# Kernel optimization log

Hardware: AMD Instinct MI355X
Metric: run time of the kernel (lower is better)

Reference implementation:

```python
import jax, jax.numpy as jnp
import numpy as np

B, S, D = 8, 2048, 2048          # batch, seq, hidden
E, K, NSTEPS = 16, 2, 4          # routed experts, top_k, routers
NSH = 2                          # shared experts
DR = D // 4                      # routed inner dim (routed_ratio=4)
DS = D // 2                      # shared inner dim (shared_ratio=2)


def setup_inputs() -> dict:
    key = jax.random.key(0)
    ks = jax.random.split(key, 8)
    s = 0.02
    return {
        "x": jax.random.normal(ks[0], (B, S, D), jnp.float32),
        "step_t": 1,
        "router_w": jax.random.normal(ks[1], (NSTEPS, D, E), jnp.float32) * s,
        "re_w1": jax.random.normal(ks[2], (E, D, DR), jnp.float32) * s,
        "re_b1": jnp.zeros((E, DR), jnp.float32),
        "re_w2": jax.random.normal(ks[3], (E, DR, D), jnp.float32) * s,
        "re_b2": jnp.zeros((E, D), jnp.float32),
        "sh_w1": jax.random.normal(ks[4], (NSH, D, DS), jnp.float32) * s,
        "sh_b1": jnp.zeros((NSH, DS), jnp.float32),
        "sh_w2": jax.random.normal(ks[5], (NSH, DS, D), jnp.float32) * s,
        "sh_b2": jnp.zeros((NSH, D), jnp.float32),
    }


def reference(x, step_t, router_w, re_w1, re_b1, re_w2, re_b2, sh_w1, sh_b1, sh_w2, sh_b2):
    orig = x.shape
    flat = x.reshape(-1, orig[-1])                       # [T, D]
    T = flat.shape[0]

    # shared expert group: sum of always-active experts
    h = jax.nn.silu(jnp.einsum('td,sdk->tsk', flat, sh_w1) + sh_b1)   # [T, NSH, DS]
    out = jnp.einsum('tsk,skd->td', h, sh_w2) + sh_b2.sum(0)          # [T, D]

    # top-k router for this step (eval mode: no jitter noise)
    logits = flat @ router_w[step_t]                     # [T, E]
    probs = jax.nn.softmax(logits, axis=-1)
    w, idx = jax.lax.top_k(probs, K)                     # [T, K]

    # combine weights per (token, expert): sum_k w_k * 1[idx_k == e]
    cw = jnp.zeros((T, E), flat.dtype).at[jnp.arange(T)[:, None], idx].add(w)

    # routed experts: masked gather-compute-scatter expressed as
    # weighted accumulation (zero combine-weight == token not routed)
    def body(acc, p):
        w1, b1, w2, b2, cwe = p                          # cwe: [T]
        ye = jax.nn.silu(flat @ w1 + b1) @ w2 + b2       # [T, D]
        return acc + cwe[:, None] * ye, None

    out, _ = jax.lax.scan(body, out, (re_w1, re_b1, re_w2, re_b2, cw.T))
    return out.reshape(orig)
```

## Files before the change

kernel.cpp:

```cpp
#include <hip/hip_runtime.h>
#include <hip/hip_bf16.h>
#include <stdint.h>


#define DEV static __device__ __forceinline__

typedef __attribute__((ext_vector_type(8))) short bf16x8;
typedef __attribute__((ext_vector_type(4))) float f32x4;

constexpr int T_TOK = 16384;
constexpr int DIM   = 2048;
constexpr int NEXP  = 16;
constexpr int DR_K  = 512;
constexpr int DS_K  = 1024;
constexpr int MAXROWS = 34816;
constexpr int MAXTILES = 272;

DEV void gload16(const void* g, void* l) {
  __builtin_amdgcn_global_load_lds(
      (const __attribute__((address_space(1))) unsigned int*)g,
      (__attribute__((address_space(3))) unsigned int*)l, 16, 0, 0);
}

DEV float silu_f(float v) { return v / (1.f + __expf(-v)); }

__global__ __launch_bounds__(256) void cast_router_kernel(
    const float* __restrict__ x, __hip_bfloat16* __restrict__ xb,
    const float* __restrict__ rw_all, const int* __restrict__ step_p,
    int* __restrict__ tk_idx, float* __restrict__ tk_w) {
  int tid = threadIdx.x;
  int t0 = blockIdx.x * 8;
  __shared__ float xs[8][1024];
  __shared__ float red[4][4][8][4];

  float acc[8][4];
#pragma unroll
  for (int tk = 0; tk < 8; ++tk)
#pragma unroll
    for (int j = 0; j < 4; ++j) acc[tk][j] = 0.f;

  const float* rwbase = rw_all + (size_t)step_p[0] * DIM * NEXP;

#pragma unroll
  for (int half = 0; half < 2; ++half) {
#pragma unroll
    for (int tk = 0; tk < 8; ++tk) {
      const float4* xp = (const float4*)(x + (size_t)(t0 + tk) * DIM + half * 1024);
      float4 v = xp[tid];
      *(float4*)&xs[tk][tid * 4] = v;
      union { ushort4 u; __hip_bfloat16 h[4]; } o;
      o.h[0] = __float2bfloat16(v.x); o.h[1] = __float2bfloat16(v.y);
      o.h[2] = __float2bfloat16(v.z); o.h[3] = __float2bfloat16(v.w);
      *(ushort4*)(xb + (size_t)(t0 + tk) * DIM + half * 1024 + tid * 4) = o.u;
    }
    __syncthreads();
    const float4* rw4 = (const float4*)(rwbase + (size_t)half * 1024 * NEXP);
#pragma unroll 4
    for (int i = 0; i < 16; ++i) {
      int c = i * 256 + tid;
      int d = c >> 2;
      float4 wv = rw4[c];
#pragma unroll
      for (int tk = 0; tk < 8; ++tk) {
        float v = xs[tk][d];
        acc[tk][0] += v * wv.x; acc[tk][1] += v * wv.y;
        acc[tk][2] += v * wv.z; acc[tk][3] += v * wv.w;
      }
    }
    __syncthreads();
  }

#pragma unroll
  for (int m = 4; m < 64; m <<= 1) {
#pragma unroll
    for (int tk = 0; tk < 8; ++tk) {
      acc[tk][0] += __shfl_xor(acc[tk][0], m);
      acc[tk][1] += __shfl_xor(acc[tk][1], m);
      acc[tk][2] += __shfl_xor(acc[tk][2], m);
      acc[tk][3] += __shfl_xor(acc[tk][3], m);
    }
  }
  int lane = tid & 63, wvi = tid >> 6;
  if (lane < 4) {
#pragma unroll
    for (int tk = 0; tk < 8; ++tk) {
      float4 r = {acc[tk][0], acc[tk][1], acc[tk][2], acc[tk][3]};
      *(float4*)&red[wvi][lane][tk][0] = r;
    }
  }
  __syncthreads();
  if (tid < 8) {
    int t = t0 + tid;
    float lg[16];
#pragma unroll
    for (int e = 0; e < 16; ++e) {
      int cg = e >> 2, j = e & 3;
      lg[e] = red[0][cg][tid][j] + red[1][cg][tid][j] +
              red[2][cg][tid][j] + red[3][cg][tid][j];
    }
    float mx = lg[0];
    for (int i = 1; i < 16; ++i) mx = fmaxf(mx, lg[i]);
    float pr[16], sum = 0.f;
    for (int i = 0; i < 16; ++i) { pr[i] = expf(lg[i] - mx); sum += pr[i]; }
    float inv = 1.f / sum;
    int b0 = -1, b1 = -1; float w0 = -1.f, w1 = -1.f;
    for (int i = 0; i < 16; ++i) {
      float v = pr[i] * inv;
      if (v > w0)      { w1 = w0; b1 = b0; w0 = v; b0 = i; }
      else if (v > w1) { w1 = v; b1 = i; }
    }
    tk_idx[2 * t] = b0; tk_idx[2 * t + 1] = b1;
    tk_w[2 * t] = w0;   tk_w[2 * t + 1] = w1;
  }
}

__global__ __launch_bounds__(256) void hist_kernel(const int* __restrict__ tk_idx,
                                                   int* __restrict__ cnt_pad) {
  __shared__ int lc[16];
  int tid = threadIdx.x;
  if (tid < 16) lc[tid] = 0;
  __syncthreads();
  int base = blockIdx.x * 2048;
#pragma unroll
  for (int i = 0; i < 8; ++i)
    atomicAdd(&lc[tk_idx[base + i * 256 + tid]], 1);
  __syncthreads();
  if (tid < 16) atomicAdd(&cnt_pad[tid * 16], lc[tid]);
}

__global__ __launch_bounds__(256) void transpose_cast(const float* __restrict__ in,
                                                      __hip_bfloat16* __restrict__ out,
                                                      int R, int C) {
  __shared__ float t[64][68];
  size_t bo = (size_t)blockIdx.z * R * C;
  in += bo; out += bo;
  int c0 = blockIdx.x * 64, r0 = blockIdx.y * 64;
  int tid = threadIdx.x;
  int rr = tid >> 2, cc0 = (tid & 3) * 16;
  const float* ip = in + (size_t)(r0 + rr) * C + c0 + cc0;
#pragma unroll
  for (int j = 0; j < 4; ++j)
    *(float4*)&t[rr][cc0 + 4 * j] = *(const float4*)(ip + 4 * j);
  __syncthreads();
  int wr = tid >> 2, wc0 = (tid & 3) * 16;
  union { bf16x8 v; __hip_bfloat16 h[8]; } o0, o1;
#pragma unroll
  for (int k = 0; k < 8; ++k) o0.h[k] = __float2bfloat16(t[wc0 + k][wr]);
#pragma unroll
  for (int k = 0; k < 8; ++k) o1.h[k] = __float2bfloat16(t[wc0 + 8 + k][wr]);
  __hip_bfloat16* op = out + (size_t)(c0 + wr) * R + r0 + wc0;
  *(bf16x8*)op = o0.v;
  *(bf16x8*)(op + 8) = o1.v;
}

__global__ void scan_kernel(const int* __restrict__ cnt_pad, int* __restrict__ seg,
                            int* __restrict__ padded, int* __restrict__ tile_e,
                            int* __restrict__ tile_m0, int* __restrict__ n_tiles) {
  if (threadIdx.x == 0) {
    int off = 0, nt = 0;
    for (int e = 0; e < NEXP; ++e) {
      seg[e] = off;
      int pc = (cnt_pad[e * 16] + 127) & ~127;
      padded[e] = pc;
      for (int m = 0; m < pc; m += 128) { tile_e[nt] = e; tile_m0[nt] = m; ++nt; }
      off += pc;
    }
    seg[NEXP] = off;
    n_tiles[0] = nt;
  }
}

__global__ __launch_bounds__(256) void scatter_kernel(
    const int* __restrict__ tk_idx, const float* __restrict__ tk_w,
    const int* __restrict__ seg, int* __restrict__ cnt2_pad,
    int* __restrict__ tok_list, float* __restrict__ w_list,
    int* __restrict__ pos_list) {
  __shared__ int lh[16], lbase[16];
  int tid = threadIdx.x;
  if (tid < 16) lh[tid] = 0;
  __syncthreads();
  int t = blockIdx.x * 256 + tid;
  int e0 = tk_idx[2 * t], e1 = tk_idx[2 * t + 1];
  int s0 = atomicAdd(&lh[e0], 1);
  int s1 = atomicAdd(&lh[e1], 1);
  __syncthreads();
  if (tid < 16) lbase[tid] = atomicAdd(&cnt2_pad[tid * 16], lh[tid]);
  __syncthreads();
  int p0 = seg[e0] + lbase[e0] + s0;
  int p1 = seg[e1] + lbase[e1] + s1;
  tok_list[p0] = t; w_list[p0] = tk_w[2 * t];     pos_list[2 * t] = p0;
  tok_list[p1] = t; w_list[p1] = tk_w[2 * t + 1]; pos_list[2 * t + 1] = p1;
}

__global__ void pad_kernel(const int* __restrict__ cnt_pad, const int* __restrict__ padded,
                           const int* __restrict__ seg, int* __restrict__ tok_list,
                           float* __restrict__ w_list) {
  int e = blockIdx.x;
  int c = cnt_pad[e * 16], pc = padded[e], s = seg[e];
  for (int i = c + threadIdx.x; i < pc; i += blockDim.x) {
    tok_list[s + i] = 0;
    w_list[s + i] = 0.f;
  }
}

DEV void swz_tile(int bid, int NB, int& tile, int& nb) {
  tile = 8 * (bid / (8 * NB)) + (bid & 7);
  nb = (bid >> 3) % NB;
}

template <int MODE>
DEV void gemm_shared(const __hip_bfloat16* __restrict__ Abase,
                     const __hip_bfloat16* __restrict__ Bt,
                     const float* __restrict__ bias,
                     __hip_bfloat16* __restrict__ outb) {
  constexpr int KD = DIM;
  constexpr int NT = KD / 64;

  int tid = threadIdx.x;
  int ln = tid & 63, w8 = tid >> 6;
  int wm = w8 >> 2, wn = w8 & 3;
  int tile, nb;
  swz_tile(blockIdx.x, 8, tile, nb);
  int m0 = tile * 256;
  int n0 = nb * 256;

  __shared__ __align__(16) char lds[2 * 65536];

  int srow = tid >> 2;
  int schunk = (tid & 3) ^ ((tid >> 3) & 3);
  int browBase;
  if constexpr (MODE == 0) {
    int s = n0 >> 10, nn = n0 & 1023;
    browBase = s * DS_K + nn;
  } else {
    browBase = n0;
  }
  const __hip_bfloat16* aS0 = Abase + (size_t)(m0 + srow) * KD + schunk * 8;
  const __hip_bfloat16* aS1 = Abase + (size_t)(m0 + 128 + srow) * KD + schunk * 8;
  const __hip_bfloat16* bS0 = Bt + (size_t)(browBase + srow) * KD + schunk * 8;
  const __hip_bfloat16* bS1 = Bt + (size_t)(browBase + 128 + srow) * KD + schunk * 8;
  int d0 = w8 * 1024;
  int d1 = 8192 + w8 * 1024;

  gload16(aS0, lds + d0);              gload16(aS1, lds + d1);
  gload16(bS0, lds + 32768 + d0);      gload16(bS1, lds + 32768 + d1);
  gload16(aS0 + 32, lds + 16384 + d0); gload16(aS1 + 32, lds + 16384 + d1);
  gload16(bS0 + 32, lds + 49152 + d0); gload16(bS1 + 32, lds + 49152 + d1);

  f32x4 acc[8][4];
#pragma unroll
  for (int i = 0; i < 8; ++i)
#pragma unroll
    for (int j = 0; j < 4; ++j) acc[i][j] = (f32x4){0.f, 0.f, 0.f, 0.f};

  int cswz = (((ln >> 4) ^ ((ln >> 1) & 3)) << 4);
  int aByte = wm * 8192 + (ln & 15) * 64 + cswz;
  int bByte = 32768 + wn * 4096 + (ln & 15) * 64 + cswz;

  bf16x8 af[4], bfr[4];

  for (int t = 0; t < NT; ++t) {
    const char* buf = lds + (t & 1) * 65536;
    char* nxt = lds + ((t + 1) & 1) * 65536;
    bool pf = (t + 1) < NT;
    int ko = (t + 1) * 64;

    asm volatile("s_waitcnt vmcnt(4)" ::: "memory");
    __builtin_amdgcn_s_barrier();

    if (pf) {
      gload16(aS0 + ko, nxt + d0);
      gload16(aS1 + ko, nxt + d1);
    }
#pragma unroll
    for (int i = 0; i < 4; ++i) af[i] = *(const bf16x8*)(buf + aByte + i * 1024);
#pragma unroll
    for (int n = 0; n < 4; ++n) bfr[n] = *(const bf16x8*)(buf + bByte + n * 1024);
    __builtin_amdgcn_s_setprio(1);
#pragma unroll
    for (int i = 0; i < 4; ++i)
#pragma unroll
      for (int n = 0; n < 4; ++n)
        acc[i][n] = __builtin_amdgcn_mfma_f32_16x16x32_bf16(af[i], bfr[n], acc[i][n], 0, 0, 0);
    __builtin_amdgcn_s_setprio(0);

    if (pf) {
      gload16(bS0 + ko, nxt + 32768 + d0);
      gload16(bS1 + ko, nxt + 32768 + d1);
    }
#pragma unroll
    for (int i = 0; i < 4; ++i) af[i] = *(const bf16x8*)(buf + aByte + (4 + i) * 1024);
    __builtin_amdgcn_s_setprio(1);
#pragma unroll
    for (int i = 0; i < 4; ++i)
#pragma unroll
      for (int n = 0; n < 4; ++n)
        acc[4 + i][n] = __builtin_amdgcn_mfma_f32_16x16x32_bf16(af[i], bfr[n], acc[4 + i][n], 0, 0, 0);
    __builtin_amdgcn_s_setprio(0);

    if (pf) asm volatile("s_waitcnt vmcnt(4)" ::: "memory");
    else    asm volatile("s_waitcnt vmcnt(0)" ::: "memory");
    __builtin_amdgcn_s_barrier();

    if (pf) {
      gload16(aS0 + ko + 32, nxt + 16384 + d0);
      gload16(aS1 + ko + 32, nxt + 16384 + d1);
    }
#pragma unroll
    for (int i = 0; i < 4; ++i) af[i] = *(const bf16x8*)(buf + 16384 + aByte + i * 1024);
#pragma unroll
    for (int n = 0; n < 4; ++n) bfr[n] = *(const bf16x8*)(buf + 16384 + bByte + n * 1024);
    __builtin_amdgcn_s_setprio(1);
#pragma unroll
    for (int i = 0; i < 4; ++i)
#pragma unroll
      for (int n = 0; n < 4; ++n)
        acc[i][n] = __builtin_amdgcn_mfma_f32_16x16x32_bf16(af[i], bfr[n], acc[i][n], 0, 0, 0);
    __builtin_amdgcn_s_setprio(0);

    if (pf) {
      gload16(bS0 + ko + 32, nxt + 49152 + d0);
      gload16(bS1 + ko + 32, nxt + 49152 + d1);
    }
#pragma unroll
    for (int i = 0; i < 4; ++i) af[i] = *(const bf16x8*)(buf + 16384 + aByte + (4 + i) * 1024);
    __builtin_amdgcn_s_setprio(1);
#pragma unroll
    for (int i = 0; i < 4; ++i)
#pragma unroll
      for (int n = 0; n < 4; ++n)
        acc[4 + i][n] = __builtin_amdgcn_mfma_f32_16x16x32_bf16(af[i], bfr[n], acc[4 + i][n], 0, 0, 0);
    __builtin_amdgcn_s_setprio(0);
  }

  int colc = ln & 15;
  int rowb = (ln >> 4) << 2;
#pragma unroll
  for (int mi = 0; mi < 8; ++mi) {
    int mlb = wm * 128 + mi * 16 + rowb;
#pragma unroll
    for (int ni = 0; ni < 4; ++ni) {
      int ng = n0 + wn * 64 + ni * 16 + colc;
#pragma unroll
      for (int j = 0; j < 4; ++j) {
        float v = acc[mi][ni][j];
        if constexpr (MODE == 0) {
          float s = silu_f(v + bias[ng]);
          outb[(size_t)(m0 + mlb + j) * 2048 + ng] = __float2bfloat16(s);
        } else {
          outb[(size_t)(m0 + mlb + j) * DIM + ng] =
              __float2bfloat16(v + bias[ng] + bias[DIM + ng]);
        }
      }
    }
  }
}

template <int MODE, int NB>
DEV void gemm_routed(const __hip_bfloat16* __restrict__ Abase,
                     const __hip_bfloat16* __restrict__ Bt,
                     const float* __restrict__ bias,
                     __hip_bfloat16* __restrict__ outb,
                     const int* __restrict__ tok_list,
                     const float* __restrict__ w_list,
                     const int* __restrict__ seg_off,
                     const int* __restrict__ tile_e,
                     const int* __restrict__ tile_m0,
                     const int* __restrict__ n_tiles) {
  constexpr int KD = (MODE == 3) ? DR_K : DIM;
  constexpr int NT = KD / 32;

  int tid = threadIdx.x;
  int ln = tid & 63, w8 = tid >> 6;
  int wm = w8 >> 2, wn = w8 & 3;

  __shared__ __align__(16) char lds[3 * 24576];
  __shared__ int tk_s[128];
  __shared__ float w_s[128];

  int W = n_tiles[0] * NB;
  int q = (W + 7) >> 3;
  int xcd = blockIdx.x & 7, k = blockIdx.x >> 3;
  if (k >= q) return;
  int w = xcd * q + k;
  if (w >= W) return;
  int tl = w / NB, nb = w % NB;

  int e = tile_e[tl];
  int m0 = tile_m0[tl];
  int n0 = nb * 256;
  int seg = seg_off[e];
  if (tid < 128) {
    if constexpr (MODE == 2) tk_s[tid] = tok_list[seg + m0 + tid];
    w_s[tid] = w_list[seg + m0 + tid];
  }
  __syncthreads();

  int srow = tid >> 2;
  int schunk = (tid & 3) ^ ((tid >> 3) & 3);
  const __hip_bfloat16 *aS, *bS0, *bS1;
  {
    int ar, br0;
    if constexpr (MODE == 2) { ar = tk_s[srow]; br0 = e * DR_K + n0 + srow; }
    else                     { ar = seg + m0 + srow; br0 = e * DIM + n0 + srow; }
    aS  = Abase + (size_t)ar * KD + schunk * 8;
    bS0 = Bt + (size_t)br0 * KD + schunk * 8;
    bS1 = bS0 + (size_t)128 * KD;
  }
  int wlds = w8 * 1024;

#pragma unroll
  for (int tt = 0; tt < 2; ++tt) {
    char* sl = lds + tt * 24576;
    int ko = tt * 32;
    gload16(aS + ko, sl + wlds);
    gload16(bS0 + ko, sl + 8192 + wlds);
    gload16(bS1 + ko, sl + 16384 + wlds);
  }
  asm volatile("s_waitcnt vmcnt(3)" ::: "memory");
  __builtin_amdgcn_s_barrier();

  f32x4 acc[4][4];
#pragma unroll
  for (int i = 0; i < 4; ++i)
#pragma unroll
    for (int j = 0; j < 4; ++j) acc[i][j] = (f32x4){0.f, 0.f, 0.f, 0.f};

  int rof = (ln & 15) * 64 + ((((ln >> 4) ^ (ln >> 1)) & 3) << 4);
  int aoffs = wm * 4096 + rof;
  int boffs = 8192 + wn * 4096 + rof;

  int s0 = 0;
  for (int t = 0; t < NT; ++t) {
    const char* sl = lds + s0 * 24576;
    int sd = s0 - 1; if (sd < 0) sd += 3;
    char* dst = lds + sd * 24576;
    bool pf = (t + 2) < NT;
    int ko = (t + 2) * 32;

    if (pf) {
      gload16(aS + ko, dst + wlds);
      gload16(bS0 + ko, dst + 8192 + wlds);
      gload16(bS1 + ko, dst + 16384 + wlds);
    }
    bf16x8 af[4], bfr[4];
#pragma unroll
    for (int fi = 0; fi < 4; ++fi)
      af[fi] = *(const bf16x8*)(sl + aoffs + fi * 1024);
#pragma unroll
    for (int ni = 0; ni < 4; ++ni)
      bfr[ni] = *(const bf16x8*)(sl + boffs + ni * 1024);
    __builtin_amdgcn_s_barrier();
    __builtin_amdgcn_s_setprio(1);
#pragma unroll
    for (int fi = 0; fi < 4; ++fi)
#pragma unroll
      for (int ni = 0; ni < 4; ++ni)
        acc[fi][ni] = __builtin_amdgcn_mfma_f32_16x16x32_bf16(af[fi], bfr[ni], acc[fi][ni], 0, 0, 0);
    __builtin_amdgcn_s_setprio(0);

    if (t + 1 < NT) {
      if (pf) asm volatile("s_waitcnt vmcnt(3)" ::: "memory");
      else    asm volatile("s_waitcnt vmcnt(0)" ::: "memory");
      __builtin_amdgcn_s_barrier();
    }
    s0 = (s0 + 1 == 3) ? 0 : s0 + 1;
  }

  int colc = ln & 15;
  int rowb = (ln >> 4) << 2;
#pragma unroll
  for (int mi = 0; mi < 4; ++mi) {
    int mlb = wm * 64 + mi * 16 + rowb;
#pragma unroll
    for (int ni = 0; ni < 4; ++ni) {
      int ng = n0 + wn * 64 + ni * 16 + colc;
#pragma unroll
      for (int j = 0; j < 4; ++j) {
        float v = acc[mi][ni][j];
        int ml = mlb + j;
        if constexpr (MODE == 2) {
          float s = silu_f(v + bias[(size_t)e * DR_K + ng]) * w_s[ml];
          outb[((size_t)seg + m0 + ml) * DR_K + ng] = __float2bfloat16(s);
        } else {
          float wv = w_s[ml];
          outb[((size_t)seg + m0 + ml) * DIM + ng] =
              __float2bfloat16(v + wv * bias[(size_t)e * DIM + ng]);
        }
      }
    }
  }
}

__global__ __launch_bounds__(512) void gemm_sh_l1(
    const __hip_bfloat16* A, const __hip_bfloat16* B, const float* bias,
    __hip_bfloat16* ob) {
  gemm_shared<0>(A, B, bias, ob);
}
__global__ __launch_bounds__(512) void gemm_sh_l2(
    const __hip_bfloat16* A, const __hip_bfloat16* B, const float* bias,
    __hip_bfloat16* ob) {
  gemm_shared<1>(A, B, bias, ob);
}
__global__ __launch_bounds__(512) void gemm_re_l1(
    const __hip_bfloat16* A, const __hip_bfloat16* B, const float* bias,
    __hip_bfloat16* ob, const int* tok, const float* wl, const int* seg,
    const int* tl_e, const int* tl_m0, const int* ntl) {
  gemm_routed<2, 2>(A, B, bias, ob, tok, wl, seg, tl_e, tl_m0, ntl);
}
__global__ __launch_bounds__(512) void gemm_re_l2(
    const __hip_bfloat16* A, const __hip_bfloat16* B, const float* bias,
    __hip_bfloat16* ob, const int* tok, const float* wl, const int* seg,
    const int* tl_e, const int* tl_m0, const int* ntl) {
  gemm_routed<3, 8>(A, B, bias, ob, tok, wl, seg, tl_e, tl_m0, ntl);
}

__global__ __launch_bounds__(256) void combine_kernel(float* __restrict__ out,
                                                      const __hip_bfloat16* __restrict__ y_sh,
                                                      const __hip_bfloat16* __restrict__ y_re,
                                                      const int* __restrict__ pos_list) {
  int t = blockIdx.x;
  int d0 = threadIdx.x << 3;
  int p0 = pos_list[2 * t], p1 = pos_list[2 * t + 1];
  union { bf16x8 v; __hip_bfloat16 h[8]; } s, a, b;
  s.v = *(const bf16x8*)(y_sh + (size_t)t * DIM + d0);
  a.v = *(const bf16x8*)(y_re + (size_t)p0 * DIM + d0);
  b.v = *(const bf16x8*)(y_re + (size_t)p1 * DIM + d0);
  float* o = out + (size_t)t * DIM + d0;
  float4 o0, o1;
  o0.x = __bfloat162float(s.h[0]) + __bfloat162float(a.h[0]) + __bfloat162float(b.h[0]);
  o0.y = __bfloat162float(s.h[1]) + __bfloat162float(a.h[1]) + __bfloat162float(b.h[1]);
  o0.z = __bfloat162float(s.h[2]) + __bfloat162float(a.h[2]) + __bfloat162float(b.h[2]);
  o0.w = __bfloat162float(s.h[3]) + __bfloat162float(a.h[3]) + __bfloat162float(b.h[3]);
  o1.x = __bfloat162float(s.h[4]) + __bfloat162float(a.h[4]) + __bfloat162float(b.h[4]);
  o1.y = __bfloat162float(s.h[5]) + __bfloat162float(a.h[5]) + __bfloat162float(b.h[5]);
  o1.z = __bfloat162float(s.h[6]) + __bfloat162float(a.h[6]) + __bfloat162float(b.h[6]);
  o1.w = __bfloat162float(s.h[7]) + __bfloat162float(a.h[7]) + __bfloat162float(b.h[7]);
  *(float4*)o = o0;
  *(float4*)(o + 4) = o1;
}

extern "C" void kernel_launch(void* const* d_in, const int* in_sizes, int n_in,
                              void* d_out, int out_size, void* d_ws, size_t ws_size,
                              hipStream_t stream) {
  const float* x     = (const float*)d_in[0];
  const int* step_p  = (const int*)d_in[1];
  const float* rw    = (const float*)d_in[2];
  const float* re_w1 = (const float*)d_in[3];
  const float* re_b1 = (const float*)d_in[4];
  const float* re_w2 = (const float*)d_in[5];
  const float* re_b2 = (const float*)d_in[6];
  const float* sh_w1 = (const float*)d_in[7];
  const float* sh_b1 = (const float*)d_in[8];
  const float* sh_w2 = (const float*)d_in[9];
  const float* sh_b2 = (const float*)d_in[10];
  float* out = (float*)d_out;

  char* w = (char*)d_ws;
  auto take = [&](size_t bytes) {
    char* p = w;
    w += (bytes + 255) & ~(size_t)255;
    return p;
  };
  __hip_bfloat16* xb     = (__hip_bfloat16*)take((size_t)T_TOK * DIM * 2);
  __hip_bfloat16* h_sh   = (__hip_bfloat16*)take((size_t)T_TOK * 2048 * 2);
  __hip_bfloat16* w1t_sh = (__hip_bfloat16*)take((size_t)2 * DS_K * DIM * 2);
  __hip_bfloat16* w2t_sh = (__hip_bfloat16*)take((size_t)DIM * 2048 * 2);
  __hip_bfloat16* h_re   = (__hip_bfloat16*)take((size_t)MAXROWS * DR_K * 2);
  __hip_bfloat16* w1t_re = (__hip_bfloat16*)take((size_t)NEXP * DR_K * DIM * 2);
  __hip_bfloat16* w2t_re = (__hip_bfloat16*)take((size_t)NEXP * DIM * DR_K * 2);
  __hip_bfloat16* y_sh   = (__hip_bfloat16*)take((size_t)T_TOK * DIM * 2);
  int* tk_idx   = (int*)take((size_t)T_TOK * 2 * 4);
  float* tk_w   = (float*)take((size_t)T_TOK * 2 * 4);
  int* ctrl     = (int*)take(4096);
  int* tok_list = (int*)take((size_t)MAXROWS * 4);
  float* w_list = (float*)take((size_t)MAXROWS * 4);
  int* pos_list = (int*)take((size_t)T_TOK * 2 * 4);
  int* tile_e   = (int*)take((size_t)MAXTILES * 4);
  int* tile_m0  = (int*)take((size_t)MAXTILES * 4);
  int* n_tiles  = (int*)take(256);
  int* cnt_pad  = ctrl;
  int* cnt2_pad = ctrl + 256;
  int* seg      = ctrl + 512;
  int* padded   = ctrl + 544;

  __hip_bfloat16* y_re = (__hip_bfloat16*)d_ws;

  hipMemsetAsync(ctrl, 0, 4096, stream);
  cast_router_kernel<<<T_TOK / 8, 256, 0, stream>>>(x, xb, rw, step_p, tk_idx, tk_w);
  transpose_cast<<<dim3(DS_K / 64, DIM / 64, 2), 256, 0, stream>>>(sh_w1, w1t_sh, DIM, DS_K);
  transpose_cast<<<dim3(DIM / 64, 2048 / 64, 1), 256, 0, stream>>>(sh_w2, w2t_sh, 2048, DIM);
  transpose_cast<<<dim3(DR_K / 64, DIM / 64, NEXP), 256, 0, stream>>>(re_w1, w1t_re, DIM, DR_K);
  transpose_cast<<<dim3(DIM / 64, DR_K / 64, NEXP), 256, 0, stream>>>(re_w2, w2t_re, DR_K, DIM);
  hist_kernel<<<16, 256, 0, stream>>>(tk_idx, cnt_pad);
  scan_kernel<<<1, 32, 0, stream>>>(cnt_pad, seg, padded, tile_e, tile_m0, n_tiles);
  scatter_kernel<<<T_TOK / 256, 256, 0, stream>>>(tk_idx, tk_w, seg, cnt2_pad,
                                                  tok_list, w_list, pos_list);
  pad_kernel<<<NEXP, 256, 0, stream>>>(cnt_pad, padded, seg, tok_list, w_list);

  gemm_sh_l1<<<64 * 8, 512, 0, stream>>>(xb, w1t_sh, sh_b1, h_sh);
  gemm_re_l1<<<MAXTILES * 2, 512, 0, stream>>>(xb, w1t_re, re_b1, h_re,
                                               tok_list, w_list, seg,
                                               tile_e, tile_m0, n_tiles);
  gemm_sh_l2<<<64 * 8, 512, 0, stream>>>(h_sh, w2t_sh, sh_b2, y_sh);
  gemm_re_l2<<<MAXTILES * 8, 512, 0, stream>>>(h_re, w2t_re, re_b2, y_re,
                                               tok_list, w_list, seg,
                                               tile_e, tile_m0, n_tiles);
  combine_kernel<<<T_TOK, 256, 0, stream>>>(out, y_sh, y_re, pos_list);
}
```

Measured before the change: 686.7 us.

## Specialize routed layer-1 GEMM with K=64 double-buffered pipeline and split prefetch

Splits the templated routed GEMM into two dedicated kernels. The layer-1 routed kernel (gathered tokens, K=2048) now processes 64-wide K steps with two 48KB LDS buffers, issuing the prefetch for the next step in two halves interleaved with the two 32-wide MFMA sub-steps, and raises wave priority around the MFMA blocks. The aim is to halve barrier and loop overhead per K and to overlap the gathered-row loads better. Layer 2 keeps the previous 3-stage 32-wide pipeline, only de-templated. The larger LDS footprint (96KB) may lower occupancy.

```diff
diff --git a/kernel.cpp b/kernel.cpp
--- a/kernel.cpp
+++ b/kernel.cpp
@@ -356,26 +356,155 @@
   }
 }
 
-template <int MODE, int NB>
-DEV void gemm_routed(const __hip_bfloat16* __restrict__ Abase,
-                     const __hip_bfloat16* __restrict__ Bt,
-                     const float* __restrict__ bias,
-                     __hip_bfloat16* __restrict__ outb,
-                     const int* __restrict__ tok_list,
-                     const float* __restrict__ w_list,
-                     const int* __restrict__ seg_off,
-                     const int* __restrict__ tile_e,
-                     const int* __restrict__ tile_m0,
-                     const int* __restrict__ n_tiles) {
-  constexpr int KD = (MODE == 3) ? DR_K : DIM;
-  constexpr int NT = KD / 32;
+__global__ __launch_bounds__(512) void gemm_re_l1(
+    const __hip_bfloat16* __restrict__ Abase,
+    const __hip_bfloat16* __restrict__ Bt,
+    const float* __restrict__ bias,
+    __hip_bfloat16* __restrict__ outb,
+    const int* __restrict__ tok_list, const float* __restrict__ w_list,
+    const int* __restrict__ seg_off, const int* __restrict__ tile_e,
+    const int* __restrict__ tile_m0, const int* __restrict__ n_tiles) {
+  constexpr int KD = DIM;
+  constexpr int NT = KD / 64;
+  constexpr int BUFSZ = 49152;
 
   int tid = threadIdx.x;
   int ln = tid & 63, w8 = tid >> 6;
   int wm = w8 >> 2, wn = w8 & 3;
 
+  __shared__ __align__(16) char lds[2 * BUFSZ];
+  __shared__ int tk_s[128];
+  __shared__ float w_s[128];
+
+  int W = n_tiles[0] * 2;
+  int q = (W + 7) >> 3;
+  int xcd = blockIdx.x & 7, k = blockIdx.x >> 3;
+  if (k >= q) return;
+  int w = xcd * q + k;
+  if (w >= W) return;
+  int tl = w >> 1, nb = w & 1;
+
+  int e = tile_e[tl];
+  int m0 = tile_m0[tl];
+  int n0 = nb * 256;
+  int seg = seg_off[e];
+  if (tid < 128) {
+    tk_s[tid] = tok_list[seg + m0 + tid];
+    w_s[tid] = w_list[seg + m0 + tid];
+  }
+  __syncthreads();
+
+  int srow = tid >> 2;
+  int schunk = (tid & 3) ^ ((tid >> 3) & 3);
+  const __hip_bfloat16* aS = Abase + (size_t)tk_s[srow] * KD + schunk * 8;
+  const __hip_bfloat16* bS0 = Bt + (size_t)(e * DR_K + n0 + srow) * KD + schunk * 8;
+  const __hip_bfloat16* bS1 = bS0 + (size_t)128 * KD;
+  int dA = w8 * 1024;
+  int dB0 = 16384 + w8 * 1024;
+  int dB1 = 16384 + 8192 + w8 * 1024;
+
+  gload16(aS, lds + dA);
+  gload16(bS0, lds + dB0);
+  gload16(bS1, lds + dB1);
+  gload16(aS + 32, lds + 8192 + dA);
+  gload16(bS0 + 32, lds + 16384 + dB0);
+  gload16(bS1 + 32, lds + 16384 + dB1);
+
+  f32x4 acc[4][4];
+#pragma unroll
+  for (int i = 0; i < 4; ++i)
+#pragma unroll
+    for (int j = 0; j < 4; ++j) acc[i][j] = (f32x4){0.f, 0.f, 0.f, 0.f};
+
+  int cswz = (((ln >> 4) ^ ((ln >> 1) & 3)) << 4);
+  int aByte = wm * 4096 + (ln & 15) * 64 + cswz;
+  int bByte = 16384 + wn * 4096 + (ln & 15) * 64 + cswz;
+
+  bf16x8 af[4], bfr[4];
+
+  for (int t = 0; t < NT; ++t) {
+    const char* buf = lds + (t & 1) * BUFSZ;
+    char* nxt = lds + ((t + 1) & 1) * BUFSZ;
+    bool pf = (t + 1) < NT;
+    int ko = (t + 1) * 64;
+
+    asm volatile("s_waitcnt vmcnt(3)" ::: "memory");
+    __builtin_amdgcn_s_barrier();
+
+    if (pf) {
+      gload16(aS + ko, nxt + dA);
+      gload16(bS0 + ko, nxt + dB0);
+      gload16(bS1 + ko, nxt + dB1);
+    }
+#pragma unroll
+    for (int i = 0; i < 4; ++i) af[i] = *(const bf16x8*)(buf + aByte + i * 1024);
+#pragma unroll
+    for (int n = 0; n < 4; ++n) bfr[n] = *(const bf16x8*)(buf + bByte + n * 1024);
+    __builtin_amdgcn_s_setprio(1);
+#pragma unroll
+    for (int i = 0; i < 4; ++i)
+#pragma unroll
+      for (int n = 0; n < 4; ++n)
+        acc[i][n] = __builtin_amdgcn_mfma_f32_16x16x32_bf16(af[i], bfr[n], acc[i][n], 0, 0, 0);
+    __builtin_amdgcn_s_setprio(0);
+
+    if (pf) asm volatile("s_waitcnt vmcnt(3)" ::: "memory");
+    else    asm volatile("s_waitcnt vmcnt(0)" ::: "memory");
+    __builtin_amdgcn_s_barrier();
+
+    if (pf) {
+      gload16(aS + ko + 32, nxt + 8192 + dA);
+      gload16(bS0 + ko + 32, nxt + 16384 + dB0);
+      gload16(bS1 + ko + 32, nxt + 16384 + dB1);
+    }
+#pragma unroll
+    for (int i = 0; i < 4; ++i) af[i] = *(const bf16x8*)(buf + 8192 + aByte + i * 1024);
+#pragma unroll
+    for (int n = 0; n < 4; ++n) bfr[n] = *(const bf16x8*)(buf + 16384 + bByte + n * 1024);
+    __builtin_amdgcn_s_setprio(1);
+#pragma unroll
+    for (int i = 0; i < 4; ++i)
+#pragma unroll
+      for (int n = 0; n < 4; ++n)
+        acc[i][n] = __builtin_amdgcn_mfma_f32_16x16x32_bf16(af[i], bfr[n], acc[i][n], 0, 0, 0);
+    __builtin_amdgcn_s_setprio(0);
+  }
+
+  int colc = ln & 15;
+  int rowb = (ln >> 4) << 2;
+#pragma unroll
+  for (int mi = 0; mi < 4; ++mi) {
+    int mlb = wm * 64 + mi * 16 + rowb;
+#pragma unroll
+    for (int ni = 0; ni < 4; ++ni) {
+      int ng = n0 + wn * 64 + ni * 16 + colc;
+#pragma unroll
+      for (int j = 0; j < 4; ++j) {
+        int ml = mlb + j;
+        float s = silu_f(acc[mi][ni][j] + bias[(size_t)e * DR_K + ng]) * w_s[ml];
+        outb[((size_t)seg + m0 + ml) * DR_K + ng] = __float2bfloat16(s);
+      }
+    }
+  }
+}
+
+__global__ __launch_bounds__(512) void gemm_re_l2(
+    const __hip_bfloat16* __restrict__ Abase,
+    const __hip_bfloat16* __restrict__ Bt,
+    const float* __restrict__ bias,
+    __hip_bfloat16* __restrict__ outb,
+    const int* __restrict__ tok_list, const float* __restrict__ w_list,
+    const int* __restrict__ seg_off, const int* __restrict__ tile_e,
+    const int* __restrict__ tile_m0, const int* __restrict__ n_tiles) {
+  constexpr int KD = DR_K;
+  constexpr int NT = KD / 32;
+  constexpr int NB = 8;
+
+  int tid = threadIdx.x;
+  int ln = tid & 63, w8 = tid >> 6;
+  int wm = w8 >> 2, wn = w8 & 3;
+
   __shared__ __align__(16) char lds[3 * 24576];
-  __shared__ int tk_s[128];
   __shared__ float w_s[128];
 
   int W = n_tiles[0] * NB;
@@ -390,23 +519,14 @@
   int m0 = tile_m0[tl];
   int n0 = nb * 256;
   int seg = seg_off[e];
-  if (tid < 128) {
-    if constexpr (MODE == 2) tk_s[tid] = tok_list[seg + m0 + tid];
-    w_s[tid] = w_list[seg + m0 + tid];
-  }
+  if (tid < 128) w_s[tid] = w_list[seg + m0 + tid];
   __syncthreads();
 
   int srow = tid >> 2;
   int schunk = (tid & 3) ^ ((tid >> 3) & 3);
-  const __hip_bfloat16 *aS, *bS0, *bS1;
-  {
-    int ar, br0;
-    if constexpr (MODE == 2) { ar = tk_s[srow]; br0 = e * DR_K + n0 + srow; }
-    else                     { ar = seg + m0 + srow; br0 = e * DIM + n0 + srow; }
-    aS  = Abase + (size_t)ar * KD + schunk * 8;
-    bS0 = Bt + (size_t)br0 * KD + schunk * 8;
-    bS1 = bS0 + (size_t)128 * KD;
-  }
+  const __hip_bfloat16* aS = Abase + (size_t)(seg + m0 + srow) * KD + schunk * 8;
+  const __hip_bfloat16* bS0 = Bt + (size_t)(e * DIM + n0 + srow) * KD + schunk * 8;
+  const __hip_bfloat16* bS1 = bS0 + (size_t)128 * KD;
   int wlds = w8 * 1024;
 
 #pragma unroll
@@ -477,16 +597,10 @@
       int ng = n0 + wn * 64 + ni * 16 + colc;
 #pragma unroll
       for (int j = 0; j < 4; ++j) {
-        float v = acc[mi][ni][j];
         int ml = mlb + j;
-        if constexpr (MODE == 2) {
-          float s = silu_f(v + bias[(size_t)e * DR_K + ng]) * w_s[ml];
-          outb[((size_t)seg + m0 + ml) * DR_K + ng] = __float2bfloat16(s);
-        } else {
-          float wv = w_s[ml];
-          outb[((size_t)seg + m0 + ml) * DIM + ng] =
-              __float2bfloat16(v + wv * bias[(size_t)e * DIM + ng]);
-        }
+        float wv = w_s[ml];
+        outb[((size_t)seg + m0 + ml) * DIM + ng] =
+            __float2bfloat16(acc[mi][ni][j] + wv * bias[(size_t)e * DIM + ng]);
       }
     }
   }
@@ -501,18 +615,6 @@
     const __hip_bfloat16* A, const __hip_bfloat16* B, const float* bias,
     __hip_bfloat16* ob) {
   gemm_shared<1>(A, B, bias, ob);
-}
-__global__ __launch_bounds__(512) void gemm_re_l1(
-    const __hip_bfloat16* A, const __hip_bfloat16* B, const float* bias,
-    __hip_bfloat16* ob, const int* tok, const float* wl, const int* seg,
-    const int* tl_e, const int* tl_m0, const int* ntl) {
-  gemm_routed<2, 2>(A, B, bias, ob, tok, wl, seg, tl_e, tl_m0, ntl);
-}
-__global__ __launch_bounds__(512) void gemm_re_l2(
-    const __hip_bfloat16* A, const __hip_bfloat16* B, const float* bias,
-    __hip_bfloat16* ob, const int* tok, const float* wl, const int* seg,
-    const int* tl_e, const int* tl_m0, const int* ntl) {
-  gemm_routed<3, 8>(A, B, bias, ob, tok, wl, seg, tl_e, tl_m0, ntl);
 }
 
 __global__ __launch_bounds__(256) void combine_kernel(float* __restrict__ out,
```

New measurement: 731.0 us. 6.5% more time.
